# Kernel optimization log

Hardware: AMD Instinct MI355X
Metric: run time of the kernel (lower is better)

Reference implementation:

```python
import jax, jax.numpy as jnp
import numpy as np
from jax import lax

B, N, C = 8, 8192, 91          # batch, num_boxes, num_classes (incl. background)
CM = C - 1                      # foreground classes
K = 1000                        # pre_nms_num_detections (per-class candidates / max per class)
MAX_TOTAL = 100                 # post_nms_num_detections
IOU_THR = 0.3
SCORE_THR = 0.0
BBOX_W = (10.0, 10.0, 5.0, 5.0)
BBOX_CLIP = float(np.log(1000.0 / 16.0))
IMG = 1024.0


def setup_inputs() -> dict:
    key = jax.random.key(0)
    k1, k2, k3, k4, k5, k6 = jax.random.split(key, 6)
    class_outputs = jax.random.normal(k1, (B, N, C), jnp.float32)
    box_outputs = jax.random.normal(k2, (B, N, C * 4), jnp.float32)
    cy = jax.random.uniform(k3, (B, N), minval=0.0, maxval=IMG)
    cx = jax.random.uniform(k4, (B, N), minval=0.0, maxval=IMG)
    sh = jax.random.uniform(k5, (B, N), minval=16.0, maxval=256.0)
    sw = jax.random.uniform(k6, (B, N), minval=16.0, maxval=256.0)
    anchor_boxes = jnp.stack([
        jnp.clip(cy - 0.5 * sh, 0.0, IMG), jnp.clip(cx - 0.5 * sw, 0.0, IMG),
        jnp.clip(cy + 0.5 * sh, 0.0, IMG), jnp.clip(cx + 0.5 * sw, 0.0, IMG)], axis=-1)
    image_info = jnp.tile(jnp.array([IMG, IMG, 1.0, 1.0], jnp.float32), (B, 1))
    return {"class_outputs": class_outputs, "box_outputs": box_outputs,
            "anchor_boxes": anchor_boxes, "image_info": image_info}


def decode_boxes(enc, anchors):
    # enc, anchors: [..., 4] (ty,tx,th,tw) / (ymin,xmin,ymax,xmax)
    wy, wx, wh, ww = BBOX_W
    ah = anchors[..., 2] - anchors[..., 0]
    aw = anchors[..., 3] - anchors[..., 1]
    acy = anchors[..., 0] + 0.5 * ah
    acx = anchors[..., 1] + 0.5 * aw
    ty = enc[..., 0] / wy
    tx = enc[..., 1] / wx
    th = jnp.minimum(enc[..., 2] / wh, BBOX_CLIP)
    tw = jnp.minimum(enc[..., 3] / ww, BBOX_CLIP)
    cy = ty * ah + acy
    cx = tx * aw + acx
    h = jnp.exp(th) * ah
    w = jnp.exp(tw) * aw
    return jnp.stack([cy - 0.5 * h, cx - 0.5 * w, cy + 0.5 * h, cx + 0.5 * w], axis=-1)


def pairwise_iou(b):  # b: [K,4] -> [K,K]
    area = jnp.maximum(b[:, 2] - b[:, 0], 0.0) * jnp.maximum(b[:, 3] - b[:, 1], 0.0)
    ih = jnp.maximum(jnp.minimum(b[:, None, 2], b[None, :, 2]) - jnp.maximum(b[:, None, 0], b[None, :, 0]), 0.0)
    iw = jnp.maximum(jnp.minimum(b[:, None, 3], b[None, :, 3]) - jnp.maximum(b[:, None, 1], b[None, :, 1]), 0.0)
    inter = ih * iw
    return inter / (area[:, None] + area[None, :] - inter + 1e-8)


def _per_class_nms(bc, sc):
    # bc: [N,4] normalized boxes, sc: [N] scores -> (kept boxes [K,4], scores [K], suppressed -> -1)
    sk, idx = lax.top_k(sc, K)
    bk = bc[idx]
    overlap = pairwise_iou(bk) > IOU_THR   # bool [K,K], sorted by score desc
    pass_thr = sk > SCORE_THR
    def body(i, keep):
        sup = jnp.any(keep & overlap[:, i])
        return keep.at[i].set(pass_thr[i] & jnp.logical_not(sup))
    keep = lax.fori_loop(0, K, body, jnp.zeros((K,), jnp.bool_))
    return bk, jnp.where(keep, sk, -1.0)


def _per_image(norm_boxes, sc):
    # norm_boxes: [N,CM,4], sc: [N,CM]
    bks, sks = jax.vmap(_per_class_nms)(jnp.transpose(norm_boxes, (1, 0, 2)), sc.T)
    fs = sks.reshape(-1)          # [CM*K]
    fb = bks.reshape(-1, 4)
    ts, ti = lax.top_k(fs, MAX_TOTAL)
    tb = fb[ti]
    tc = (ti // K).astype(jnp.float32)   # 0-based fg class index
    valid = ts > SCORE_THR
    ts = jnp.where(valid, ts, 0.0)
    tb = jnp.where(valid[:, None], tb, 0.0)
    tc = jnp.where(valid, tc, 0.0)
    return tb, ts, tc, jnp.sum(valid).astype(jnp.int32)


def reference(class_outputs, box_outputs, anchor_boxes, image_info):
    probs = jax.nn.softmax(class_outputs, axis=-1)
    scores = probs[..., 1:]                                   # [B,N,CM]
    enc = box_outputs.reshape(B, N, C, 4)[:, :, 1:, :]        # [B,N,CM,4]
    anchors = jnp.broadcast_to(anchor_boxes[:, :, None, :], (B, N, CM, 4))
    boxes = decode_boxes(enc, anchors)                        # [B,N,CM,4]
    h = image_info[:, 0]
    w = image_info[:, 1]
    hw = jnp.stack([h, w, h, w], axis=-1)                     # [B,4]
    boxes = jnp.clip(boxes, 0.0, hw[:, None, None, :])        # clip to image
    norm_boxes = boxes / hw[:, None, None, :]                 # to_normalized_coordinates
    pb, ps, pc, nv = lax.map(lambda a: _per_image(*a), (norm_boxes, scores))
    post_boxes = pb * hw[:, None, :]                          # to_absolute_coordinates
    post_classes = pc + 1.0                                   # shift back over background
    return (nv, post_boxes, post_classes, ps)
```

## Files before the change

kernel.cpp:

```cpp
#include <hip/hip_runtime.h>
#include <math.h>

#define Bb 8
#define Nn 8192
#define Cc 91
#define CM 90
#define Kk 1000
#define MAXT 100
#define KSEL 256
#define NW 4
#define IOU_THR 0.3f
#define BBOX_CLIP 4.135166556742356f
#define IMG 1024.0f
#define SM_ROWS 64

typedef unsigned long long u64;
typedef unsigned int u32;

__global__ __launch_bounds__(64) void softmax_scores(
    const float* __restrict__ cls, float* __restrict__ scores_t) {
    __shared__ float rowbuf[SM_ROWS * Cc];
    int blk = blockIdx.x;
    int lane = threadIdx.x;
    const float4* src = (const float4*)(cls + (size_t)blk * SM_ROWS * Cc);
    for (int i = lane; i < SM_ROWS * Cc / 4; i += 64) {
        float4 v = src[i];
        *(float4*)&rowbuf[i * 4] = v;
    }
    __syncthreads();
    int row_g = blk * SM_ROWS + lane;
    int b = row_g >> 13;
    int n = row_g & (Nn - 1);
    const float* row = &rowbuf[lane * Cc];
    float m = row[0];
    for (int c = 1; c < Cc; c++) m = fmaxf(m, row[c]);
    float s = 0.0f;
    for (int c = 0; c < Cc; c++) s += expf(row[c] - m);
    for (int c = 1; c < Cc; c++) {
        float p = expf(row[c] - m) / s;
        scores_t[((size_t)(b * CM + (c - 1))) * Nn + n] = p;
    }
}

__global__ __launch_bounds__(512) void topk_nms(
    const float* __restrict__ scores_t,
    const float* __restrict__ box_out, const float* __restrict__ anchors,
    u64* __restrict__ cand_key, float* __restrict__ cand_box) {
    __shared__ __align__(16) char smem[45840];
    u32* sbits = (u32*)smem;
    int (*whist)[256] = (int(*)[256])(smem + 32768);
    u64* keys  = (u64*)(smem + 40960);
    float4* kb = (float4*)(smem + 43008);
    float* kar = (float*)(smem + 44608);
    u64* kkey  = (u64*)(smem + 45008);
    int* scal  = (int*)(smem + 45808);
    int* rksc  = (int*)(smem + 32768);
    u64* keys2 = (u64*)(smem + 36864);
    int* eqidx = (int*)(smem + 38912);
    float* dy1 = (float*)(smem);
    float* dx1 = (float*)(smem + 1024);
    float* dy2 = (float*)(smem + 2048);
    float* dx2 = (float*)(smem + 3072);
    float* dar = (float*)(smem + 4096);
    #define sh_need  scal[0]
    #define sh_digit scal[1]
    #define sh_cnt   scal[2]
    #define sh_eq    scal[3]
    #define sh_kcnt  scal[4]

    int bc = blockIdx.x;
    int b = bc / CM;
    int c = bc % CM;
    int tid = threadIdx.x;
    int wave = tid >> 6, lane = tid & 63;

    const float4* s4 = (const float4*)(scores_t + (size_t)bc * Nn);
    for (int i = tid; i < Nn / 4; i += 512) {
        float4 v = s4[i];
        sbits[i * 4 + 0] = __float_as_uint(v.x);
        sbits[i * 4 + 1] = __float_as_uint(v.y);
        sbits[i * 4 + 2] = __float_as_uint(v.z);
        sbits[i * 4 + 3] = __float_as_uint(v.w);
    }
    if (tid == 0) { sh_need = KSEL; sh_cnt = 0; sh_eq = 0; }
    __syncthreads();

    u32 prefix = 0;
    int hi = 32;
    for (int p = 0; p < 4; p++) {
        int lo = hi - 8;
        for (int i = tid; i < 8 * 256; i += 512) ((int*)whist)[i] = 0;
        __syncthreads();
        if (p == 0) {
            for (int i = tid; i < Nn; i += 512) {
                u32 d = sbits[i] >> 24;
                u64 active = ~0ull;
                while (active) {
                    int leader = __ffsll(active) - 1;
                    u32 dl = (u32)__shfl((int)d, leader);
                    u64 mm = __ballot(d == dl);
                    if (lane == leader)
                        atomicAdd(&whist[wave][dl], (int)__popcll(mm & active));
                    active &= ~mm;
                }
            }
        } else {
            for (int i = tid; i < Nn; i += 512) {
                u32 v = sbits[i];
                if ((v >> hi) == prefix)
                    atomicAdd(&whist[wave][(v >> lo) & 255], 1);
            }
        }
        __syncthreads();
        if (tid < 256) {
            int h = 0;
            for (int w = 0; w < 8; w++) h += whist[w][tid];
            whist[0][tid] = h;
        }
        __syncthreads();
        if (wave == 0) {
            int4 hb = *(const int4*)&whist[0][4 * lane];
            int tl = hb.x + hb.y + hb.z + hb.w;
            int run = tl;
            for (int off = 1; off < 64; off <<= 1) {
                int v = __shfl_down(run, off, 64);
                if (lane + off < 64) run += v;
            }
            int sa = run - tl;
            int need = sh_need;
            if (need > sa && need <= sa + tl) {
                int s3 = sa + hb.w;
                int s2 = s3 + hb.z;
                int s1 = s2 + hb.y;
                int d, nn;
                if (s3 >= need)      { d = 4 * lane + 3; nn = need - sa; }
                else if (s2 >= need) { d = 4 * lane + 2; nn = need - s3; }
                else if (s1 >= need) { d = 4 * lane + 1; nn = need - s2; }
                else                 { d = 4 * lane + 0; nn = need - s1; }
                sh_digit = d;
                sh_need = nn;
            }
        }
        __syncthreads();
        prefix = (prefix << 8) | (u32)sh_digit;
        hi = lo;
        __syncthreads();
    }
    u32 Tb = prefix;
    int m = sh_need;

    for (int i = tid; i < Nn; i += 512) {
        u32 v = sbits[i];
        if (v > Tb) {
            int pp = atomicAdd(&sh_cnt, 1);
            keys[pp] = ((u64)v << 13) | (u64)(8191 - i);
        } else if (v == Tb) {
            int pp = atomicAdd(&sh_eq, 1);
            if (pp < 256) eqidx[pp] = i;
        }
    }
    __syncthreads();
    if (tid == 0) {
        int e = min(sh_eq, 256);
        for (int t = 0; t < m; t++) {
            int best = -1, bi = 0x7FFFFFFF;
            for (int q = 0; q < e; q++) {
                int ii = eqidx[q];
                if (ii < bi) { bi = ii; best = q; }
            }
            if (best >= 0) {
                eqidx[best] = 0x7FFFFFFF;
                int pp = atomicAdd(&sh_cnt, 1);
                keys[pp] = ((u64)Tb << 13) | (u64)(8191 - bi);
            }
        }
    }
    __syncthreads();

    {
        int t = tid & 255;
        int hf = tid >> 8;
        u64 my = keys[t];
        int base = hf << 7;
        int cnt = 0;
        #pragma unroll 8
        for (int q = 0; q < 128; q++)
            cnt += (keys[base + q] > my) ? 1 : 0;
        rksc[hf * 256 + t] = cnt;
    }
    __syncthreads();
    if (tid < 256) {
        int r = rksc[tid] + rksc[256 + tid];
        keys2[r] = keys[tid];
    }
    __syncthreads();

    if (tid < KSEL) {
        u64 key = keys2[tid];
        int n = 8191 - (int)(key & 0x1FFF);
        const float4 e = *(const float4*)(box_out + ((size_t)(b * Nn + n)) * (Cc * 4) + (size_t)(c + 1) * 4);
        const float4 a = *(const float4*)(anchors + (size_t)(b * Nn + n) * 4);
        float ah = a.z - a.x, aw = a.w - a.y;
        float acy = a.x + 0.5f * ah, acx = a.y + 0.5f * aw;
        float ty = e.x / 10.0f, tx = e.y / 10.0f;
        float th = fminf(e.z / 5.0f, BBOX_CLIP);
        float tw = fminf(e.w / 5.0f, BBOX_CLIP);
        float cy = ty * ah + acy, cx = tx * aw + acx;
        float h = expf(th) * ah, w = expf(tw) * aw;
        float y1 = cy - 0.5f * h, x1 = cx - 0.5f * w;
        float y2 = cy + 0.5f * h, x2 = cx + 0.5f * w;
        y1 = fminf(fmaxf(y1, 0.0f), IMG) * (1.0f / IMG);
        x1 = fminf(fmaxf(x1, 0.0f), IMG) * (1.0f / IMG);
        y2 = fminf(fmaxf(y2, 0.0f), IMG) * (1.0f / IMG);
        x2 = fminf(fmaxf(x2, 0.0f), IMG) * (1.0f / IMG);
        float area = fmaxf(y2 - y1, 0.0f) * fmaxf(x2 - x1, 0.0f);
        dy1[tid] = y1; dx1[tid] = x1;
        dy2[tid] = y2; dx2[tid] = x2;
        dar[tid] = area;
    }
    __syncthreads();

    if (tid < 64) {
        int kcnt = 0;
        for (int ci = 0; ci < NW && kcnt < MAXT; ci++) {
            int i = ci * 64 + lane;
            u64 key = keys2[i];
            float sc = __uint_as_float((u32)(key >> 13));
            float y1 = dy1[i], x1 = dx1[i];
            float y2 = dy2[i], x2 = dx2[i];
            float area = dar[i];

            bool sup = false;
            for (int r = 0; r < kcnt; r++) {
                float4 kv = kb[r];
                float ka = kar[r];
                float ih = fmaxf(fminf(kv.z, y2) - fmaxf(kv.x, y1), 0.0f);
                float iw = fmaxf(fminf(kv.w, x2) - fmaxf(kv.y, x1), 0.0f);
                float inter = ih * iw;
                sup = sup | (inter > IOU_THR * (ka + area - inter + 1e-8f));
            }
            u64 rem = __ballot((sc > 0.0f) && !sup);
            while (rem != 0ull && kcnt < MAXT) {
                int j = __ffsll(rem) - 1;
                rem &= rem - 1;
                float jy1 = __shfl(y1, j), jx1 = __shfl(x1, j);
                float jy2 = __shfl(y2, j), jx2 = __shfl(x2, j);
                float jar = __shfl(area, j);
                if (lane == j) {
                    kb[kcnt] = make_float4(y1, x1, y2, x2);
                    kar[kcnt] = area;
                    int flat = c * Kk + i;
                    kkey[kcnt] = ((u64)__float_as_uint(sc) << 32)
                               | ((u64)(u32)(131071 - flat) << 14)
                               | (u64)(u32)(c * MAXT + kcnt);
                }
                float ih = fmaxf(fminf(jy2, y2) - fmaxf(jy1, y1), 0.0f);
                float iw = fmaxf(fminf(jx2, x2) - fmaxf(jx1, x1), 0.0f);
                float inter = ih * iw;
                bool ov = inter > IOU_THR * (jar + area - inter + 1e-8f);
                u64 mm = __ballot(ov);
                rem &= ~mm;
                kcnt++;
            }
        }
        if (lane == 0) sh_kcnt = kcnt;
    }
    __syncthreads();

    int kcnt = sh_kcnt;
    for (int r = tid; r < MAXT; r += 512) {
        int slot = bc * MAXT + r;
        if (r < kcnt) {
            cand_key[slot] = kkey[r];
            float4 v = kb[r];
            cand_box[slot * 4 + 0] = v.x;
            cand_box[slot * 4 + 1] = v.y;
            cand_box[slot * 4 + 2] = v.z;
            cand_box[slot * 4 + 3] = v.w;
        } else {
            cand_key[slot] = 0ull;
        }
    }
    #undef sh_need
    #undef sh_digit
    #undef sh_cnt
    #undef sh_eq
    #undef sh_kcnt
}

__global__ __launch_bounds__(256) void final_topk(
    const u64* __restrict__ cand_key, const float* __restrict__ cand_box,
    float* __restrict__ out) {
    extern __shared__ u64 sk[];
    __shared__ u64 res[MAXT];
    int b = blockIdx.x;
    int tid = threadIdx.x;

    for (int i = tid; i < CM * MAXT; i += 256)
        sk[i] = cand_key[b * CM * MAXT + i];
    __syncthreads();

    if (tid < 64) {
        int lane = tid;
        int c0 = lane, c1 = lane + 64;
        bool h1 = c1 < CM;
        int p0 = 0, p1 = 0;
        u64 k0 = sk[c0 * MAXT + 0];
        u64 k0n = sk[c0 * MAXT + 1];
        u64 k1 = h1 ? sk[c1 * MAXT + 0] : 0ull;
        u64 k1n = h1 ? sk[c1 * MAXT + 1] : 0ull;
        for (int t = 0; t < MAXT; t++) {
            u64 m = (k0 > k1) ? k0 : k1;
            for (int off = 32; off > 0; off >>= 1) {
                u64 o = __shfl_xor(m, off);
                if (o > m) m = o;
            }
            if (lane == 0) res[t] = m;
            if (m != 0ull) {
                if (m == k0) {
                    p0++; k0 = k0n;
                    k0n = (p0 + 1 < MAXT) ? sk[c0 * MAXT + p0 + 1] : 0ull;
                } else if (h1 && m == k1) {
                    p1++; k1 = k1n;
                    k1n = (p1 + 1 < MAXT) ? sk[c1 * MAXT + p1 + 1] : 0ull;
                }
            }
        }
    }
    __syncthreads();

    for (int t = tid; t < MAXT; t += 256) {
        u64 m = res[t];
        float sc = __uint_as_float((u32)(m >> 32));
        bool valid = sc > 0.0f;
        float b0 = 0.f, b1 = 0.f, b2 = 0.f, b3 = 0.f, clsv = 0.f, sv = 0.f;
        if (valid) {
            int idx = (int)(m & 0x3FFF);
            int slot = b * CM * MAXT + idx;
            b0 = cand_box[slot * 4 + 0] * IMG;
            b1 = cand_box[slot * 4 + 1] * IMG;
            b2 = cand_box[slot * 4 + 2] * IMG;
            b3 = cand_box[slot * 4 + 3] * IMG;
            clsv = (float)(idx / MAXT + 1);
            sv = sc;
        }
        int o = (b * MAXT + t);
        out[8 + o * 4 + 0] = b0;
        out[8 + o * 4 + 1] = b1;
        out[8 + o * 4 + 2] = b2;
        out[8 + o * 4 + 3] = b3;
        out[8 + Bb * MAXT * 4 + o] = clsv;
        out[8 + Bb * MAXT * 5 + o] = sv;
    }
    if (tid == 0) {
        int nv = 0;
        for (int t = 0; t < MAXT; t++) nv += ((res[t] >> 32) != 0ull) ? 1 : 0;
        out[b] = (float)nv;
    }
}

extern "C" void kernel_launch(void* const* d_in, const int* in_sizes, int n_in,
                              void* d_out, int out_size, void* d_ws, size_t ws_size,
                              hipStream_t stream) {
    (void)in_sizes; (void)n_in; (void)out_size; (void)ws_size;
    const float* cls  = (const float*)d_in[0];
    const float* boxo = (const float*)d_in[1];
    const float* anch = (const float*)d_in[2];
    float* out = (float*)d_out;
    char* ws = (char*)d_ws;

    float* scores_t = (float*)(ws);
    u64*   cand_key = (u64*)  (ws + 23592960);
    float* cand_box = (float*)(ws + 24168960);

    softmax_scores<<<(Bb * Nn) / SM_ROWS, 64, 0, stream>>>(cls, scores_t);
    topk_nms<<<Bb * CM, 512, 0, stream>>>(scores_t, boxo, anch, cand_key, cand_box);
    final_topk<<<Bb, 256, CM * MAXT * sizeof(u64), stream>>>(cand_key, cand_box, out);
}
```

Before: 268.4 us.

## Restructure radix select into 8/12/12-bit passes and fuse rank sort with decode

The four 8-bit radix-select passes become three passes. The first is an 8-bit histogram built during the score load, and the other two are 12-bit passes using a 4096-bin shared histogram with a two-level scan. The separate rank-counting sort stage is folded into the box-decode step, so each selected thread ranks its own key and writes the decoded box straight to its sorted slot. The aim is fewer barriers and passes over the 8192 scores in shared memory. In exchange, shared memory use grows and the first-pass atomics see more contention on the top byte.

New measurement: 262.4 us. 2.2% less time.

```diff
diff --git a/kernel.cpp b/kernel.cpp
--- a/kernel.cpp
+++ b/kernel.cpp
@@ -46,22 +46,23 @@
     const float* __restrict__ scores_t,
     const float* __restrict__ box_out, const float* __restrict__ anchors,
     u64* __restrict__ cand_key, float* __restrict__ cand_box) {
-    __shared__ __align__(16) char smem[45840];
-    u32* sbits = (u32*)smem;
-    int (*whist)[256] = (int(*)[256])(smem + 32768);
-    u64* keys  = (u64*)(smem + 40960);
+    __shared__ __align__(16) char smem[53408];
+    u32* sbits   = (u32*)smem;
+    int* hist1   = (int*)(smem + 32768);
+    int* whist0f = (int*)(smem + 49152);
+    int* part    = (int*)(smem + 49152);
+    int* scal    = (int*)(smem + 53376);
+    u64* keys  = (u64*)(smem + 32768);
+    int* eqidx = (int*)(smem + 34816);
+    u64* keys2 = (u64*)(smem + 35840);
+    float* dy1 = (float*)(smem + 37888);
+    float* dx1 = (float*)(smem + 38912);
+    float* dy2 = (float*)(smem + 39936);
+    float* dx2 = (float*)(smem + 40960);
+    float* dar = (float*)(smem + 41984);
     float4* kb = (float4*)(smem + 43008);
     float* kar = (float*)(smem + 44608);
     u64* kkey  = (u64*)(smem + 45008);
-    int* scal  = (int*)(smem + 45808);
-    int* rksc  = (int*)(smem + 32768);
-    u64* keys2 = (u64*)(smem + 36864);
-    int* eqidx = (int*)(smem + 38912);
-    float* dy1 = (float*)(smem);
-    float* dx1 = (float*)(smem + 1024);
-    float* dy2 = (float*)(smem + 2048);
-    float* dx2 = (float*)(smem + 3072);
-    float* dar = (float*)(smem + 4096);
     #define sh_need  scal[0]
     #define sh_digit scal[1]
     #define sh_cnt   scal[2]
@@ -74,79 +75,140 @@
     int tid = threadIdx.x;
     int wave = tid >> 6, lane = tid & 63;
 
+    #pragma unroll
+    for (int i = 0; i < 8; i++) hist1[tid + 512 * i] = 0;
+    for (int i = tid; i < 8 * 132; i += 512) whist0f[i] = 0;
+    if (tid == 0) { sh_need = KSEL; sh_cnt = 0; sh_eq = 0; }
+    __syncthreads();
+
     const float4* s4 = (const float4*)(scores_t + (size_t)bc * Nn);
+    int* myrow = &whist0f[wave * 132];
     for (int i = tid; i < Nn / 4; i += 512) {
         float4 v = s4[i];
-        sbits[i * 4 + 0] = __float_as_uint(v.x);
-        sbits[i * 4 + 1] = __float_as_uint(v.y);
-        sbits[i * 4 + 2] = __float_as_uint(v.z);
-        sbits[i * 4 + 3] = __float_as_uint(v.w);
-    }
-    if (tid == 0) { sh_need = KSEL; sh_cnt = 0; sh_eq = 0; }
-    __syncthreads();
-
-    u32 prefix = 0;
-    int hi = 32;
-    for (int p = 0; p < 4; p++) {
-        int lo = hi - 8;
-        for (int i = tid; i < 8 * 256; i += 512) ((int*)whist)[i] = 0;
-        __syncthreads();
-        if (p == 0) {
-            for (int i = tid; i < Nn; i += 512) {
-                u32 d = sbits[i] >> 24;
-                u64 active = ~0ull;
-                while (active) {
-                    int leader = __ffsll(active) - 1;
-                    u32 dl = (u32)__shfl((int)d, leader);
-                    u64 mm = __ballot(d == dl);
-                    if (lane == leader)
-                        atomicAdd(&whist[wave][dl], (int)__popcll(mm & active));
-                    active &= ~mm;
-                }
-            }
-        } else {
-            for (int i = tid; i < Nn; i += 512) {
-                u32 v = sbits[i];
-                if ((v >> hi) == prefix)
-                    atomicAdd(&whist[wave][(v >> lo) & 255], 1);
-            }
-        }
-        __syncthreads();
-        if (tid < 256) {
-            int h = 0;
-            for (int w = 0; w < 8; w++) h += whist[w][tid];
-            whist[0][tid] = h;
-        }
-        __syncthreads();
-        if (wave == 0) {
-            int4 hb = *(const int4*)&whist[0][4 * lane];
-            int tl = hb.x + hb.y + hb.z + hb.w;
-            int run = tl;
-            for (int off = 1; off < 64; off <<= 1) {
-                int v = __shfl_down(run, off, 64);
-                if (lane + off < 64) run += v;
-            }
-            int sa = run - tl;
-            int need = sh_need;
-            if (need > sa && need <= sa + tl) {
-                int s3 = sa + hb.w;
-                int s2 = s3 + hb.z;
-                int s1 = s2 + hb.y;
-                int d, nn;
-                if (s3 >= need)      { d = 4 * lane + 3; nn = need - sa; }
-                else if (s2 >= need) { d = 4 * lane + 2; nn = need - s3; }
-                else if (s1 >= need) { d = 4 * lane + 1; nn = need - s2; }
-                else                 { d = 4 * lane + 0; nn = need - s1; }
-                sh_digit = d;
-                sh_need = nn;
-            }
-        }
-        __syncthreads();
-        prefix = (prefix << 8) | (u32)sh_digit;
-        hi = lo;
-        __syncthreads();
-    }
-    u32 Tb = prefix;
+        u32 x0 = __float_as_uint(v.x), x1 = __float_as_uint(v.y);
+        u32 x2 = __float_as_uint(v.z), x3 = __float_as_uint(v.w);
+        sbits[i * 4 + 0] = x0;
+        sbits[i * 4 + 1] = x1;
+        sbits[i * 4 + 2] = x2;
+        sbits[i * 4 + 3] = x3;
+        atomicAdd(&myrow[x0 >> 24], 1);
+        atomicAdd(&myrow[x1 >> 24], 1);
+        atomicAdd(&myrow[x2 >> 24], 1);
+        atomicAdd(&myrow[x3 >> 24], 1);
+    }
+    __syncthreads();
+
+    if (tid < 128) {
+        int h = 0;
+        #pragma unroll
+        for (int w = 0; w < 8; w++) h += whist0f[w * 132 + tid];
+        part[tid] = h;
+    }
+    __syncthreads();
+    if (wave == 0) {
+        int c0 = part[2 * lane], c1 = part[2 * lane + 1];
+        int tl = c0 + c1;
+        int run = tl;
+        for (int off = 1; off < 64; off <<= 1) {
+            int v = __shfl_down(run, off, 64);
+            if (lane + off < 64) run += v;
+        }
+        int sa = run - tl;
+        int need0 = sh_need;
+        if (need0 > sa && need0 <= sa + tl) {
+            if (sa + c1 >= need0) { sh_digit = 2 * lane + 1; sh_need = need0 - sa; }
+            else                  { sh_digit = 2 * lane;     sh_need = need0 - (sa + c1); }
+        }
+    }
+    __syncthreads();
+    u32 P8 = (u32)sh_digit;
+
+    for (int i = tid; i < Nn; i += 512) {
+        u32 v = sbits[i];
+        if ((v >> 24) == P8) atomicAdd(&hist1[(v >> 12) & 4095], 1);
+    }
+    __syncthreads();
+    {
+        int s = 0;
+        #pragma unroll
+        for (int q = 0; q < 8; q++) s += hist1[tid * 8 + q];
+        part[tid] = s;
+    }
+    __syncthreads();
+    if (wave == 0) {
+        int gsum = 0;
+        #pragma unroll
+        for (int q = 0; q < 8; q++) gsum += part[lane * 8 + q];
+        int run = gsum;
+        for (int off = 1; off < 64; off <<= 1) {
+            int v = __shfl_down(run, off, 64);
+            if (lane + off < 64) run += v;
+        }
+        int sa = run - gsum;
+        int need0 = sh_need;
+        bool hit = (need0 > sa) && (need0 <= sa + gsum);
+        u64 mk = __ballot(hit);
+        int g = __ffsll(mk) - 1;
+        int sabase = __shfl(sa, g);
+        int cj = hist1[64 * g + lane];
+        int run2 = cj;
+        for (int off = 1; off < 64; off <<= 1) {
+            int v = __shfl_down(run2, off, 64);
+            if (lane + off < 64) run2 += v;
+        }
+        int sa2 = sabase + (run2 - cj);
+        if (need0 > sa2 && need0 <= sa2 + cj) {
+            sh_digit = 64 * g + lane;
+            sh_need = need0 - sa2;
+        }
+    }
+    __syncthreads();
+    u32 P20 = (P8 << 12) | (u32)sh_digit;
+
+    #pragma unroll
+    for (int i = 0; i < 8; i++) hist1[tid + 512 * i] = 0;
+    __syncthreads();
+    for (int i = tid; i < Nn; i += 512) {
+        u32 v = sbits[i];
+        if ((v >> 12) == P20) atomicAdd(&hist1[v & 4095], 1);
+    }
+    __syncthreads();
+    {
+        int s = 0;
+        #pragma unroll
+        for (int q = 0; q < 8; q++) s += hist1[tid * 8 + q];
+        part[tid] = s;
+    }
+    __syncthreads();
+    if (wave == 0) {
+        int gsum = 0;
+        #pragma unroll
+        for (int q = 0; q < 8; q++) gsum += part[lane * 8 + q];
+        int run = gsum;
+        for (int off = 1; off < 64; off <<= 1) {
+            int v = __shfl_down(run, off, 64);
+            if (lane + off < 64) run += v;
+        }
+        int sa = run - gsum;
+        int need0 = sh_need;
+        bool hit = (need0 > sa) && (need0 <= sa + gsum);
+        u64 mk = __ballot(hit);
+        int g = __ffsll(mk) - 1;
+        int sabase = __shfl(sa, g);
+        int cj = hist1[64 * g + lane];
+        int run2 = cj;
+        for (int off = 1; off < 64; off <<= 1) {
+            int v = __shfl_down(run2, off, 64);
+            if (lane + off < 64) run2 += v;
+        }
+        int sa2 = sabase + (run2 - cj);
+        if (need0 > sa2 && need0 <= sa2 + cj) {
+            sh_digit = 64 * g + lane;
+            sh_need = need0 - sa2;
+        }
+    }
+    __syncthreads();
+    u32 Tb = (P20 << 12) | (u32)sh_digit;
     int m = sh_need;
 
     for (int i = tid; i < Nn; i += 512) {
@@ -177,29 +239,15 @@
     }
     __syncthreads();
 
-    {
-        int t = tid & 255;
-        int hf = tid >> 8;
-        u64 my = keys[t];
-        int base = hf << 7;
-        int cnt = 0;
-        #pragma unroll 8
-        for (int q = 0; q < 128; q++)
-            cnt += (keys[base + q] > my) ? 1 : 0;
-        rksc[hf * 256 + t] = cnt;
-    }
-    __syncthreads();
-    if (tid < 256) {
-        int r = rksc[tid] + rksc[256 + tid];
-        keys2[r] = keys[tid];
-    }
-    __syncthreads();
-
     if (tid < KSEL) {
-        u64 key = keys2[tid];
-        int n = 8191 - (int)(key & 0x1FFF);
+        u64 my = keys[tid];
+        int n = 8191 - (int)(my & 0x1FFF);
         const float4 e = *(const float4*)(box_out + ((size_t)(b * Nn + n)) * (Cc * 4) + (size_t)(c + 1) * 4);
         const float4 a = *(const float4*)(anchors + (size_t)(b * Nn + n) * 4);
+        int r = 0;
+        #pragma unroll 8
+        for (int q = 0; q < KSEL; q++) r += (keys[q] > my) ? 1 : 0;
+        keys2[r] = my;
         float ah = a.z - a.x, aw = a.w - a.y;
         float acy = a.x + 0.5f * ah, acx = a.y + 0.5f * aw;
         float ty = e.x / 10.0f, tx = e.y / 10.0f;
@@ -214,9 +262,9 @@
         y2 = fminf(fmaxf(y2, 0.0f), IMG) * (1.0f / IMG);
         x2 = fminf(fmaxf(x2, 0.0f), IMG) * (1.0f / IMG);
         float area = fmaxf(y2 - y1, 0.0f) * fmaxf(x2 - x1, 0.0f);
-        dy1[tid] = y1; dx1[tid] = x1;
-        dy2[tid] = y2; dx2[tid] = x2;
-        dar[tid] = area;
+        dy1[r] = y1; dx1[r] = x1;
+        dy2[r] = y2; dx2[r] = x2;
+        dar[r] = area;
     }
     __syncthreads();
 
```

## Switch radix select to 12/10/10-bit passes and fuse rank-sort with box decode

Applied to the files above, without the earlier changes.

Replaces the four 8-bit radix-select passes, which used per-wave histograms and a wave-aggregated atomic first pass, with three passes of 12, 10 and 10 bits over a single shared 1024-bin histogram. The first pass is fused with the global load of the scores. The two-phase rank-count sort plus scatter is merged into the box-decode step: each thread ranks its key against all 256 and writes its decoded box directly at the rank position. Shared memory is relaid out and shrunk, which cuts barriers and passes over the score array. The trade-off is more atomic contention on a single histogram and a longer serial rank loop per thread.

After: 252.5 us. 5.9% less time.

```diff
diff --git a/kernel.cpp b/kernel.cpp
--- a/kernel.cpp
+++ b/kernel.cpp
@@ -46,22 +46,21 @@
     const float* __restrict__ scores_t,
     const float* __restrict__ box_out, const float* __restrict__ anchors,
     u64* __restrict__ cand_key, float* __restrict__ cand_box) {
-    __shared__ __align__(16) char smem[45840];
+    __shared__ __align__(16) char smem[36896];
     u32* sbits = (u32*)smem;
-    int (*whist)[256] = (int(*)[256])(smem + 32768);
-    u64* keys  = (u64*)(smem + 40960);
-    float4* kb = (float4*)(smem + 43008);
-    float* kar = (float*)(smem + 44608);
-    u64* kkey  = (u64*)(smem + 45008);
-    int* scal  = (int*)(smem + 45808);
-    int* rksc  = (int*)(smem + 32768);
-    u64* keys2 = (u64*)(smem + 36864);
-    int* eqidx = (int*)(smem + 38912);
-    float* dy1 = (float*)(smem);
-    float* dx1 = (float*)(smem + 1024);
-    float* dy2 = (float*)(smem + 2048);
-    float* dx2 = (float*)(smem + 3072);
-    float* dar = (float*)(smem + 4096);
+    int* hist  = (int*)(smem + 32768);
+    int* scal  = (int*)(smem + 36864);
+    u64* keys  = (u64*)(smem + 32768);
+    int* eqidx = (int*)(smem + 34816);
+    u64* keys2 = (u64*)(smem);
+    float* dy1 = (float*)(smem + 2048);
+    float* dx1 = (float*)(smem + 3072);
+    float* dy2 = (float*)(smem + 4096);
+    float* dx2 = (float*)(smem + 5120);
+    float* dar = (float*)(smem + 6144);
+    float4* kb = (float4*)(smem + 7168);
+    float* kar = (float*)(smem + 8768);
+    u64* kkey  = (u64*)(smem + 9168);
     #define sh_need  scal[0]
     #define sh_digit scal[1]
     #define sh_cnt   scal[2]
@@ -74,89 +73,115 @@
     int tid = threadIdx.x;
     int wave = tid >> 6, lane = tid & 63;
 
+    hist[tid] = 0;
+    hist[tid + 512] = 0;
+    if (tid == 0) { sh_need = KSEL; sh_cnt = 0; sh_eq = 0; }
+    __syncthreads();
+
     const float4* s4 = (const float4*)(scores_t + (size_t)bc * Nn);
+    float4 v0 = s4[tid];
+    float4 v1 = s4[tid + 512];
+    float4 v2 = s4[tid + 1024];
+    float4 v3 = s4[tid + 1536];
+    u32 x[16];
+    x[0]  = __float_as_uint(v0.x); x[1]  = __float_as_uint(v0.y);
+    x[2]  = __float_as_uint(v0.z); x[3]  = __float_as_uint(v0.w);
+    x[4]  = __float_as_uint(v1.x); x[5]  = __float_as_uint(v1.y);
+    x[6]  = __float_as_uint(v1.z); x[7]  = __float_as_uint(v1.w);
+    x[8]  = __float_as_uint(v2.x); x[9]  = __float_as_uint(v2.y);
+    x[10] = __float_as_uint(v2.z); x[11] = __float_as_uint(v2.w);
+    x[12] = __float_as_uint(v3.x); x[13] = __float_as_uint(v3.y);
+    x[14] = __float_as_uint(v3.z); x[15] = __float_as_uint(v3.w);
+    *(uint4*)&sbits[(tid)        * 4] = make_uint4(x[0], x[1], x[2], x[3]);
+    *(uint4*)&sbits[(tid + 512)  * 4] = make_uint4(x[4], x[5], x[6], x[7]);
+    *(uint4*)&sbits[(tid + 1024) * 4] = make_uint4(x[8], x[9], x[10], x[11]);
+    *(uint4*)&sbits[(tid + 1536) * 4] = make_uint4(x[12], x[13], x[14], x[15]);
+    #pragma unroll
+    for (int k = 0; k < 16; k++) atomicAdd(&hist[x[k] >> 20], 1);
+    __syncthreads();
+
+    #define SELECT_DIGIT()                                                   \
+    if (wave == 0) {                                                         \
+        int4 h0 = *(const int4*)&hist[16 * lane];                            \
+        int4 h1 = *(const int4*)&hist[16 * lane + 4];                        \
+        int4 h2 = *(const int4*)&hist[16 * lane + 8];                        \
+        int4 h3 = *(const int4*)&hist[16 * lane + 12];                       \
+        int cnt[16] = {h0.x, h0.y, h0.z, h0.w, h1.x, h1.y, h1.z, h1.w,       \
+                       h2.x, h2.y, h2.z, h2.w, h3.x, h3.y, h3.z, h3.w};      \
+        int gsum = 0;                                                        \
+        _Pragma("unroll")                                                    \
+        for (int j = 0; j < 16; j++) gsum += cnt[j];                         \
+        int run = gsum;                                                      \
+        for (int off = 1; off < 64; off <<= 1) {                             \
+            int vv = __shfl_down(run, off, 64);                              \
+            if (lane + off < 64) run += vv;                                  \
+        }                                                                    \
+        int sa = run - gsum;                                                 \
+        int need = sh_need;                                                  \
+        if (need > sa && need <= sa + gsum) {                                \
+            int acc = sa;                                                    \
+            _Pragma("unroll")                                                \
+            for (int j = 15; j >= 0; j--) {                                  \
+                if (acc + cnt[j] >= need) {                                  \
+                    sh_digit = 16 * lane + j;                                \
+                    sh_need = need - acc;                                    \
+                    break;                                                   \
+                }                                                            \
+                acc += cnt[j];                                               \
+            }                                                                \
+        }                                                                    \
+    }
+
+    SELECT_DIGIT();
+    __syncthreads();
+    u32 P12 = (u32)sh_digit;
+
+    hist[tid] = 0;
+    hist[tid + 512] = 0;
+    __syncthreads();
     for (int i = tid; i < Nn / 4; i += 512) {
-        float4 v = s4[i];
-        sbits[i * 4 + 0] = __float_as_uint(v.x);
-        sbits[i * 4 + 1] = __float_as_uint(v.y);
-        sbits[i * 4 + 2] = __float_as_uint(v.z);
-        sbits[i * 4 + 3] = __float_as_uint(v.w);
-    }
-    if (tid == 0) { sh_need = KSEL; sh_cnt = 0; sh_eq = 0; }
-    __syncthreads();
-
-    u32 prefix = 0;
-    int hi = 32;
-    for (int p = 0; p < 4; p++) {
-        int lo = hi - 8;
-        for (int i = tid; i < 8 * 256; i += 512) ((int*)whist)[i] = 0;
-        __syncthreads();
-        if (p == 0) {
-            for (int i = tid; i < Nn; i += 512) {
-                u32 d = sbits[i] >> 24;
-                u64 active = ~0ull;
-                while (active) {
-                    int leader = __ffsll(active) - 1;
-                    u32 dl = (u32)__shfl((int)d, leader);
-                    u64 mm = __ballot(d == dl);
-                    if (lane == leader)
-                        atomicAdd(&whist[wave][dl], (int)__popcll(mm & active));
-                    active &= ~mm;
-                }
-            }
-        } else {
-            for (int i = tid; i < Nn; i += 512) {
-                u32 v = sbits[i];
-                if ((v >> hi) == prefix)
-                    atomicAdd(&whist[wave][(v >> lo) & 255], 1);
-            }
-        }
-        __syncthreads();
-        if (tid < 256) {
-            int h = 0;
-            for (int w = 0; w < 8; w++) h += whist[w][tid];
-            whist[0][tid] = h;
-        }
-        __syncthreads();
-        if (wave == 0) {
-            int4 hb = *(const int4*)&whist[0][4 * lane];
-            int tl = hb.x + hb.y + hb.z + hb.w;
-            int run = tl;
-            for (int off = 1; off < 64; off <<= 1) {
-                int v = __shfl_down(run, off, 64);
-                if (lane + off < 64) run += v;
-            }
-            int sa = run - tl;
-            int need = sh_need;
-            if (need > sa && need <= sa + tl) {
-                int s3 = sa + hb.w;
-                int s2 = s3 + hb.z;
-                int s1 = s2 + hb.y;
-                int d, nn;
-                if (s3 >= need)      { d = 4 * lane + 3; nn = need - sa; }
-                else if (s2 >= need) { d = 4 * lane + 2; nn = need - s3; }
-                else if (s1 >= need) { d = 4 * lane + 1; nn = need - s2; }
-                else                 { d = 4 * lane + 0; nn = need - s1; }
-                sh_digit = d;
-                sh_need = nn;
-            }
-        }
-        __syncthreads();
-        prefix = (prefix << 8) | (u32)sh_digit;
-        hi = lo;
-        __syncthreads();
-    }
-    u32 Tb = prefix;
+        uint4 v = *(const uint4*)&sbits[i * 4];
+        if ((v.x >> 20) == P12) atomicAdd(&hist[(v.x >> 10) & 1023], 1);
+        if ((v.y >> 20) == P12) atomicAdd(&hist[(v.y >> 10) & 1023], 1);
+        if ((v.z >> 20) == P12) atomicAdd(&hist[(v.z >> 10) & 1023], 1);
+        if ((v.w >> 20) == P12) atomicAdd(&hist[(v.w >> 10) & 1023], 1);
+    }
+    __syncthreads();
+    SELECT_DIGIT();
+    __syncthreads();
+    u32 P22 = (P12 << 10) | (u32)sh_digit;
+
+    hist[tid] = 0;
+    hist[tid + 512] = 0;
+    __syncthreads();
+    for (int i = tid; i < Nn / 4; i += 512) {
+        uint4 v = *(const uint4*)&sbits[i * 4];
+        if ((v.x >> 10) == P22) atomicAdd(&hist[v.x & 1023], 1);
+        if ((v.y >> 10) == P22) atomicAdd(&hist[v.y & 1023], 1);
+        if ((v.z >> 10) == P22) atomicAdd(&hist[v.z & 1023], 1);
+        if ((v.w >> 10) == P22) atomicAdd(&hist[v.w & 1023], 1);
+    }
+    __syncthreads();
+    SELECT_DIGIT();
+    __syncthreads();
+    u32 Tb = (P22 << 10) | (u32)sh_digit;
     int m = sh_need;
-
-    for (int i = tid; i < Nn; i += 512) {
-        u32 v = sbits[i];
-        if (v > Tb) {
-            int pp = atomicAdd(&sh_cnt, 1);
-            keys[pp] = ((u64)v << 13) | (u64)(8191 - i);
-        } else if (v == Tb) {
-            int pp = atomicAdd(&sh_eq, 1);
-            if (pp < 256) eqidx[pp] = i;
+    #undef SELECT_DIGIT
+
+    for (int i = tid; i < Nn / 4; i += 512) {
+        uint4 v4 = *(const uint4*)&sbits[i * 4];
+        u32 vs[4] = {v4.x, v4.y, v4.z, v4.w};
+        #pragma unroll
+        for (int k = 0; k < 4; k++) {
+            u32 v = vs[k];
+            int idx = i * 4 + k;
+            if (v > Tb) {
+                int pp = atomicAdd(&sh_cnt, 1);
+                keys[pp] = ((u64)v << 13) | (u64)(8191 - idx);
+            } else if (v == Tb) {
+                int pp = atomicAdd(&sh_eq, 1);
+                if (pp < 256) eqidx[pp] = idx;
+            }
         }
     }
     __syncthreads();
@@ -177,29 +202,15 @@
     }
     __syncthreads();
 
-    {
-        int t = tid & 255;
-        int hf = tid >> 8;
-        u64 my = keys[t];
-        int base = hf << 7;
-        int cnt = 0;
-        #pragma unroll 8
-        for (int q = 0; q < 128; q++)
-            cnt += (keys[base + q] > my) ? 1 : 0;
-        rksc[hf * 256 + t] = cnt;
-    }
-    __syncthreads();
-    if (tid < 256) {
-        int r = rksc[tid] + rksc[256 + tid];
-        keys2[r] = keys[tid];
-    }
-    __syncthreads();
-
     if (tid < KSEL) {
-        u64 key = keys2[tid];
-        int n = 8191 - (int)(key & 0x1FFF);
+        u64 my = keys[tid];
+        int n = 8191 - (int)(my & 0x1FFF);
         const float4 e = *(const float4*)(box_out + ((size_t)(b * Nn + n)) * (Cc * 4) + (size_t)(c + 1) * 4);
         const float4 a = *(const float4*)(anchors + (size_t)(b * Nn + n) * 4);
+        int r = 0;
+        #pragma unroll 8
+        for (int q = 0; q < KSEL; q++) r += (keys[q] > my) ? 1 : 0;
+        keys2[r] = my;
         float ah = a.z - a.x, aw = a.w - a.y;
         float acy = a.x + 0.5f * ah, acx = a.y + 0.5f * aw;
         float ty = e.x / 10.0f, tx = e.y / 10.0f;
@@ -214,9 +225,9 @@
         y2 = fminf(fmaxf(y2, 0.0f), IMG) * (1.0f / IMG);
         x2 = fminf(fmaxf(x2, 0.0f), IMG) * (1.0f / IMG);
         float area = fmaxf(y2 - y1, 0.0f) * fmaxf(x2 - x1, 0.0f);
-        dy1[tid] = y1; dx1[tid] = x1;
-        dy2[tid] = y2; dx2[tid] = x2;
-        dar[tid] = area;
+        dy1[r] = y1; dx1[r] = x1;
+        dy2[r] = y2; dx2[r] = x2;
+        dar[r] = area;
     }
     __syncthreads();
 
```
